# Kernel tuning notes

Measured on AMD Instinct MI355X. Metric: run time of the kernel, lower is better.

## Reference

```python
import jax, jax.numpy as jnp
import numpy as np
import math

D_MSA, N_HEAD, D_HID = 256, 8, 32
B, N, L = 1, 256, 384


def _xavier(key, shape):
    fan_in, fan_out = shape[1], shape[0]
    a = math.sqrt(6.0 / (fan_in + fan_out))
    return jax.random.uniform(key, shape, jnp.float32, -a, a)


def setup_inputs() -> dict:
    key = jax.random.key(0)
    ks = jax.random.split(key, 8)
    hd = N_HEAD * D_HID
    return {
        "msa": jax.random.normal(ks[0], (B, N, L, D_MSA), jnp.float32),
        "ln_w": jnp.ones((D_MSA,), jnp.float32),
        "ln_b": jnp.zeros((D_MSA,), jnp.float32),
        # torch Linear weight is [out, in]; y = x @ W.T
        "wq": _xavier(ks[1], (hd, D_MSA)),
        "wk": _xavier(ks[2], (hd, D_MSA)),
        "wv": _xavier(ks[3], (hd, D_MSA)),
        # to_g init: zeros weight, ones bias -> randomize a bit for nontrivial test
        "wg": 0.02 * jax.random.normal(ks[4], (hd, D_MSA), jnp.float32),
        "bg": jnp.ones((hd,), jnp.float32),
        "wo": 0.02 * jax.random.normal(ks[5], (D_MSA, hd), jnp.float32),
        "bo": jnp.zeros((D_MSA,), jnp.float32),
    }


def reference(msa, ln_w, ln_b, wq, wk, wv, wg, bg, wo, bo):
    h, d = N_HEAD, D_HID
    scaling = 1.0 / math.sqrt(d)
    b, n, l, dm = msa.shape

    # LayerNorm over last dim
    mu = jnp.mean(msa, axis=-1, keepdims=True)
    var = jnp.var(msa, axis=-1, keepdims=True)
    x = (msa - mu) / jnp.sqrt(var + 1e-5) * ln_w + ln_b

    q = (x @ wq.T).reshape(b, n, l, h, d) * scaling
    k = (x @ wk.T).reshape(b, n, l, h, d)
    v = (x @ wv.T).reshape(b, n, l, h, d)
    gate = jax.nn.sigmoid(x @ wg.T + bg)  # [b,n,l,h*d]

    # column-wise attention: softmax over MSA sequence axis N (keys)
    attn = jnp.einsum("bqihd,bkihd->bihqk", q, k)  # [b,l,h,n,n]
    attn = jax.nn.softmax(attn, axis=-1)
    out = jnp.einsum("bihqk,bkihd->bqihd", attn, v).reshape(b, n, l, h * d)
    out = gate * out
    return out @ wo.T + bo
```

## Files before the change

### kernel.cpp

```cpp
#include <hip/hip_runtime.h>

typedef unsigned short u16;
typedef unsigned int u32;
typedef __attribute__((ext_vector_type(8))) short bf16x8;
typedef __attribute__((ext_vector_type(4))) float f32x4;
typedef __attribute__((ext_vector_type(4))) u32 u32x4;

#define N_SEQ 256
#define L_RES 384
#define DM 256
#define NH 8
#define DH 32
#define M_ROWS (N_SEQ*L_RES)
#define PANEL 8192


__device__ __forceinline__ u16 f2b(float f){
    unsigned u = __builtin_bit_cast(unsigned, f);
    u = u + 0x7fffu + ((u >> 16) & 1u);
    return (u16)(u >> 16);
}
__device__ __forceinline__ float b2f(u16 b){
    unsigned u = ((unsigned)b) << 16;
    return __builtin_bit_cast(float, u);
}
__device__ __forceinline__ u32 pk2(float lo, float hi){
    u32 a = (__builtin_bit_cast(u32, lo) + 0x8000u) >> 16;
    u32 b = (__builtin_bit_cast(u32, hi) + 0x8000u) & 0xffff0000u;
    return a | b;
}
__device__ __forceinline__ int swzB(int a){
    return a ^ (((a>>6)&7)<<3);
}

__global__ __launch_bounds__(256) void k_wcvt(const float* __restrict__ wq,
        const float* __restrict__ wk, const float* __restrict__ wv,
        const float* __restrict__ wg, const float* __restrict__ wo,
        u16* __restrict__ wsw){
    const int mat = blockIdx.x >> 6;
    const float* W = (mat==0)?wq:(mat==1)?wk:(mat==2)?wv:(mat==3)?wg:wo;
    const int r = ((blockIdx.x & 63)*256 + threadIdx.x)*4;
    const int col = r >> 8, k0 = r & 255;
    float4 f = *(const float4*)&W[r];
    ushort4 o;
    o.x = f2b(f.x); o.y = f2b(f.y); o.z = f2b(f.z); o.w = f2b(f.w);
    const int off = ((col>>4)*32 + (k0>>3))*128 + (col&15)*8 + (k0&7);
    *(ushort4*)&wsw[mat*65536 + off] = o;
}

__global__ __launch_bounds__(256) void k_ln(const float* __restrict__ msa,
        const float* __restrict__ lnw, const float* __restrict__ lnb,
        u16* __restrict__ xo){
    const int tid = threadIdx.x;
    const int r16 = tid >> 4, lane16 = tid & 15;
    const size_t row = (size_t)blockIdx.x*16 + r16;
    const float4* src = (const float4*)(msa + row*DM + lane16*16);
    float4 a[4];
    float s = 0.f, ss = 0.f;
    #pragma unroll
    for(int j=0;j<4;j++){
        a[j] = src[j];
        s  += a[j].x + a[j].y + a[j].z + a[j].w;
        ss += a[j].x*a[j].x + a[j].y*a[j].y + a[j].z*a[j].z + a[j].w*a[j].w;
    }
    #pragma unroll
    for(int m=1;m<16;m<<=1){ s += __shfl_xor(s,m); ss += __shfl_xor(ss,m); }
    const float mu  = s*(1.f/DM);
    const float inv = rsqrtf(ss*(1.f/DM) - mu*mu + 1e-5f);
    const float4* wv4 = (const float4*)(lnw + lane16*16);
    const float4* bv4 = (const float4*)(lnb + lane16*16);
    u32 pk[8];
    #pragma unroll
    for(int j=0;j<4;j++){
        float4 w = wv4[j], b = bv4[j];
        float e0 = (a[j].x-mu)*inv*w.x + b.x;
        float e1 = (a[j].y-mu)*inv*w.y + b.y;
        float e2 = (a[j].z-mu)*inv*w.z + b.z;
        float e3 = (a[j].w-mu)*inv*w.w + b.w;
        pk[j*2]   = (u32)f2b(e0) | ((u32)f2b(e1)<<16);
        pk[j*2+1] = (u32)f2b(e2) | ((u32)f2b(e3)<<16);
    }
    u16* base = xo + (size_t)blockIdx.x*4096 + lane16*256 + r16*8;
    *(uint4*)base       = *(uint4*)&pk[0];
    *(uint4*)(base+128) = *(uint4*)&pk[4];
}

__global__ __launch_bounds__(512) void k_qkvg(const u16* __restrict__ x,
        const u16* __restrict__ wsw, const float* __restrict__ bg,
        u16* __restrict__ qo, u16* __restrict__ ko,
        u16* __restrict__ vo, u16* __restrict__ go){
    __shared__ __align__(16) u16 Bs[16384];
    const int by = blockIdx.x, mat = blockIdx.y;
    const int tid = threadIdx.x;
    const int w = tid>>6, lane = tid&63, l15 = lane&15, lq = lane>>4;
    const u16* xa = x + ((size_t)by*8 + w)*4096;
    bf16x8 xf[8];
    #pragma unroll
    for(int kk=0;kk<8;kk++)
        xf[kk] = *(const bf16x8*)&xa[(kk*4+lq)*128 + l15*8];
    const float scaling = 0.17677669529663687f * 1.44269504088896f;
    u16* O = (mat==0)?qo:(mat==1)?ko:(mat==2)?vo:go;
    const int n0 = by/3, l0 = (by%3)*128;
    const int l = l0 + w*16 + l15;
    #pragma unroll 1
    for(int cg=0; cg<4; ++cg){
        const u16* wt = wsw + mat*65536 + cg*16384;
        __syncthreads();
        #pragma unroll
        for(int i=0;i<4;i++)
            *(uint4*)&Bs[swzB(i*4096 + tid*8)] = *(const uint4*)&wt[i*4096 + tid*8];
        __syncthreads();
        f32x4 acc[4] = {};
        #pragma unroll
        for(int kk=0;kk<8;kk++){
            #pragma unroll
            for(int nt=0;nt<4;nt++){
                bf16x8 b = *(const bf16x8*)&Bs[swzB(nt*4096 + (kk*4+lq)*128 + l15*8)];
                acc[nt] = __builtin_amdgcn_mfma_f32_16x16x32_bf16(b,xf[kk],acc[nt],0,0,0);
            }
        }
        #pragma unroll
        for(int nt=0;nt<4;nt++){
            const int c = cg*64 + nt*16 + lq*4;
            float v0 = acc[nt][0], v1 = acc[nt][1];
            float v2 = acc[nt][2], v3 = acc[nt][3];
            if(mat==0){ v0*=scaling; v1*=scaling; v2*=scaling; v3*=scaling; }
            else if(mat==3){
                const float4 bgv = *(const float4*)&bg[c];
                v0 = 1.f/(1.f+__expf(-(v0+bgv.x)));
                v1 = 1.f/(1.f+__expf(-(v1+bgv.y)));
                v2 = 1.f/(1.f+__expf(-(v2+bgv.z)));
                v3 = 1.f/(1.f+__expf(-(v3+bgv.w)));
            }
            uint2 ov;
            ov.x = pk2(v0, v1);
            ov.y = pk2(v2, v3);
            const int h2 = c >> 5, d = c & 31;
            *(uint2*)&O[((size_t)l*NH + h2)*PANEL + n0*32 + d] = ov;
        }
    }
}

__global__ __launch_bounds__(512, 4) void k_attn(const u16* __restrict__ q,
        const u16* __restrict__ k, const u16* __restrict__ v,
        const u16* __restrict__ g, u16* __restrict__ ao){
    __shared__ __align__(16) u16 KFs[8192];
    __shared__ __align__(16) u16 VFs[8192];
    const int h = blockIdx.x, l = blockIdx.y;
    const int tid = threadIdx.x;
    const size_t pbase = ((size_t)l*NH + h)*PANEL;
    const u16* kp = k + pbase;
    const u16* vp = v + pbase;
    #pragma unroll
    for(int j=0;j<2;j++){
        const int u = j*512 + tid;
        const int key = u>>2, dblk = u&3;
        const uint4 tk = *(const uint4*)&kp[u*8];
        *(uint4*)&KFs[((key>>4)*4 + dblk)*128 + (key&15)*8] = tk;
        const uint4 tv = *(const uint4*)&vp[u*8];
        const int T = key>>4, gg = (key>>2)&3, r = key&3;
        const int pkey = (T>>1)*32 + ((gg&2)|(T&1))*8 + r + (((gg^T)&1)<<2);
        const int plo = (pkey>>3)*128 + (pkey&7);
        const u32 wv_[4] = {tv.x, tv.y, tv.z, tv.w};
        #pragma unroll
        for(int wd=0; wd<4; wd++){
            const int d_lo = dblk*8 + wd*2, d_hi = d_lo+1;
            VFs[((d_lo)>>4)*4096 + plo + ((d_lo)&15)*8] = (u16)(wv_[wd]&0xffff);
            VFs[((d_hi)>>4)*4096 + plo + ((d_hi)&15)*8] = (u16)(wv_[wd]>>16);
        }
    }
    __syncthreads();
    const int w = tid>>6, lane = tid&63;
    const int l15 = lane&15, lq = lane>>4;
    const int lodd = lq & 1;
    const u16* qp = q + pbase;
    const u16* gp = g + pbase;
    u16* aop = ao + pbase;
    const int q0a = w*32, q0b = w*32 + 16;
    const bf16x8 bqA = *(const bf16x8*)&qp[(q0a+l15)*32 + lq*8];
    const bf16x8 bqB = *(const bf16x8*)&qp[(q0b+l15)*32 + lq*8];
    float mA = -1e30f, spA = 0.f;
    float mB = -1e30f, spB = 0.f;
    f32x4 oaccA[2] = {}, oaccB[2] = {};
    #pragma unroll
    for(int ch=0; ch<4; ch++){
        f32x4 sA[4], sB[4];
        #pragma unroll
        for(int tt=0;tt<4;tt++){
            bf16x8 ak = *(const bf16x8*)&KFs[((ch*4+tt)*4 + lq)*128 + l15*8];
            f32x4 z = {};
            sA[tt] = __builtin_amdgcn_mfma_f32_16x16x32_bf16(ak,bqA,z,0,0,0);
            f32x4 z2 = {};
            sB[tt] = __builtin_amdgcn_mfma_f32_16x16x32_bf16(ak,bqB,z2,0,0,0);
        }
        float cmA = fmaxf(fmaxf(fmaxf(sA[0][0],sA[0][1]),fmaxf(sA[0][2],sA[0][3])),
                   fmaxf(fmaxf(fmaxf(sA[1][0],sA[1][1]),fmaxf(sA[1][2],sA[1][3])),
                   fmaxf(fmaxf(fmaxf(sA[2][0],sA[2][1]),fmaxf(sA[2][2],sA[2][3])),
                         fmaxf(fmaxf(sA[3][0],sA[3][1]),fmaxf(sA[3][2],sA[3][3])))));
        float cmB = fmaxf(fmaxf(fmaxf(sB[0][0],sB[0][1]),fmaxf(sB[0][2],sB[0][3])),
                   fmaxf(fmaxf(fmaxf(sB[1][0],sB[1][1]),fmaxf(sB[1][2],sB[1][3])),
                   fmaxf(fmaxf(fmaxf(sB[2][0],sB[2][1]),fmaxf(sB[2][2],sB[2][3])),
                         fmaxf(fmaxf(sB[3][0],sB[3][1]),fmaxf(sB[3][2],sB[3][3])))));
        cmA = fmaxf(cmA, __shfl_xor(cmA,16));
        cmB = fmaxf(cmB, __shfl_xor(cmB,16));
        cmA = fmaxf(cmA, __shfl_xor(cmA,32));
        cmB = fmaxf(cmB, __shfl_xor(cmB,32));
        if(!__all((cmA <= mA + 8.f) && (cmB <= mB + 8.f))){
            const float mnA = fmaxf(mA, cmA), mnB = fmaxf(mB, cmB);
            const float scA = exp2f(mA - mnA), scB = exp2f(mB - mnB);
            mA = mnA; mB = mnB;
            spA *= scA; spB *= scB;
            #pragma unroll
            for(int i=0;i<4;i++){ oaccA[0][i]*=scA; oaccA[1][i]*=scA; oaccB[0][i]*=scB; oaccB[1][i]*=scB; }
        }
        float csA = 0.f, csB = 0.f;
        #pragma unroll
        for(int tt=0;tt<4;tt++){
            #pragma unroll
            for(int rg=0;rg<4;rg++){
                float eA = exp2f(sA[tt][rg] - mA);
                float eB = exp2f(sB[tt][rg] - mB);
                sA[tt][rg] = eA; csA += eA;
                sB[tt][rg] = eB; csB += eB;
            }
        }
        spA += csA;
        spB += csB;
        #pragma unroll
        for(int half=0; half<2; half++){
            const int mwin = ch*2 + half;
            u32 eA0 = pk2(sA[half*2][0],   sA[half*2][1]);
            u32 eA1 = pk2(sA[half*2][2],   sA[half*2][3]);
            u32 oA0 = pk2(sA[half*2+1][0], sA[half*2+1][1]);
            u32 oA1 = pk2(sA[half*2+1][2], sA[half*2+1][3]);
            u32 eB0 = pk2(sB[half*2][0],   sB[half*2][1]);
            u32 eB1 = pk2(sB[half*2][2],   sB[half*2][3]);
            u32 oB0 = pk2(sB[half*2+1][0], sB[half*2+1][1]);
            u32 oB1 = pk2(sB[half*2+1][2], sB[half*2+1][3]);
            u32 ownA0 = lodd ? oA0 : eA0,  ownA1 = lodd ? oA1 : eA1;
            u32 sndA0 = lodd ? eA0 : oA0,  sndA1 = lodd ? eA1 : oA1;
            u32 ownB0 = lodd ? oB0 : eB0,  ownB1 = lodd ? oB1 : eB1;
            u32 sndB0 = lodd ? eB0 : oB0,  sndB1 = lodd ? eB1 : oB1;
            u32 rcA0 = (u32)__shfl_xor((int)sndA0, 16);
            u32 rcB0 = (u32)__shfl_xor((int)sndB0, 16);
            u32 rcA1 = (u32)__shfl_xor((int)sndA1, 16);
            u32 rcB1 = (u32)__shfl_xor((int)sndB1, 16);
            u32x4 pwA = {ownA0, ownA1, rcA0, rcA1};
            u32x4 pwB = {ownB0, ownB1, rcB0, rcB1};
            bf16x8 pfA = __builtin_bit_cast(bf16x8, pwA);
            bf16x8 pfB = __builtin_bit_cast(bf16x8, pwB);
            #pragma unroll
            for(int nt=0;nt<2;nt++){
                bf16x8 av = *(const bf16x8*)&VFs[(nt*32 + mwin*4 + lq)*128 + l15*8];
                oaccA[nt] = __builtin_amdgcn_mfma_f32_16x16x32_bf16(av,pfA,oaccA[nt],0,0,0);
                oaccB[nt] = __builtin_amdgcn_mfma_f32_16x16x32_bf16(av,pfB,oaccB[nt],0,0,0);
            }
        }
    }
    spA += __shfl_xor(spA, 16);
    spB += __shfl_xor(spB, 16);
    spA += __shfl_xor(spA, 32);
    spB += __shfl_xor(spB, 32);
    const float rinvA = 1.f/spA, rinvB = 1.f/spB;
    const int qnA = q0a + l15, qnB = q0b + l15;
    #pragma unroll
    for(int nt=0;nt<2;nt++){
        const int c = nt*16 + lq*4;
        const uint2 glA = *(const uint2*)&gp[qnA*32 + c];
        const uint2 glB = *(const uint2*)&gp[qnB*32 + c];
        uint2 ovA, ovB;
        ovA.x = pk2(b2f((u16)(glA.x&0xffff))*oaccA[nt][0]*rinvA,
                    b2f((u16)(glA.x>>16))   *oaccA[nt][1]*rinvA);
        ovA.y = pk2(b2f((u16)(glA.y&0xffff))*oaccA[nt][2]*rinvA,
                    b2f((u16)(glA.y>>16))   *oaccA[nt][3]*rinvA);
        ovB.x = pk2(b2f((u16)(glB.x&0xffff))*oaccB[nt][0]*rinvB,
                    b2f((u16)(glB.x>>16))   *oaccB[nt][1]*rinvB);
        ovB.y = pk2(b2f((u16)(glB.y&0xffff))*oaccB[nt][2]*rinvB,
                    b2f((u16)(glB.y>>16))   *oaccB[nt][3]*rinvB);
        *(uint2*)&aop[qnA*32 + c] = ovA;
        *(uint2*)&aop[qnB*32 + c] = ovB;
    }
}

__global__ __launch_bounds__(512) void k_out(const u16* __restrict__ a,
        const u16* __restrict__ wsw, const float* __restrict__ bo,
        float* __restrict__ out){
    __shared__ __align__(16) u16 Bs[16384];
    const int cb = blockIdx.x, nb = blockIdx.y, l = blockIdx.z;
    const int c0 = cb*64;
    const int tid = threadIdx.x;
    const u16* wt = wsw + 4*65536 + (c0>>4)*4096;
    #pragma unroll
    for(int i=0;i<4;i++)
        *(uint4*)&Bs[swzB(i*4096 + tid*8)] = *(const uint4*)&wt[i*4096 + tid*8];
    const int w = tid>>6, lane = tid&63, l15 = lane&15, lq = lane>>4;
    const int n0 = nb*128 + w*16;
    const size_t lbase = (size_t)l*NH*PANEL;
    bf16x8 af[8];
    #pragma unroll
    for(int kk=0;kk<8;kk++)
        af[kk] = *(const bf16x8*)&a[lbase + (size_t)kk*PANEL + (n0 + l15)*32 + lq*8];
    __syncthreads();
    f32x4 acc[4] = {};
    #pragma unroll
    for(int kk=0;kk<8;kk++){
        #pragma unroll
        for(int nt=0;nt<4;nt++){
            bf16x8 b = *(const bf16x8*)&Bs[swzB(nt*4096 + (kk*4+lq)*128 + l15*8)];
            acc[nt] = __builtin_amdgcn_mfma_f32_16x16x32_bf16(af[kk],b,acc[nt],0,0,0);
        }
    }
    #pragma unroll
    for(int nt=0;nt<4;nt++){
        const int c = c0 + nt*16 + l15;
        const float bov = bo[c];
        #pragma unroll
        for(int rg=0;rg<4;rg++){
            const int n = n0 + lq*4 + rg;
            out[((size_t)n*L_RES + l)*DM + c] = acc[nt][rg] + bov;
        }
    }
}

extern "C" void kernel_launch(void* const* d_in, const int* in_sizes, int n_in,
                              void* d_out, int out_size, void* d_ws, size_t ws_size,
                              hipStream_t stream){
    const float* msa = (const float*)d_in[0];
    const float* lnw = (const float*)d_in[1];
    const float* lnb = (const float*)d_in[2];
    const float* wq  = (const float*)d_in[3];
    const float* wk  = (const float*)d_in[4];
    const float* wv  = (const float*)d_in[5];
    const float* wg  = (const float*)d_in[6];
    const float* bg  = (const float*)d_in[7];
    const float* wo  = (const float*)d_in[8];
    const float* bo  = (const float*)d_in[9];
    float* out = (float*)d_out;

    const size_t SEG = (size_t)M_ROWS * DM;
    u16 *xs, *qs, *ks, *vs, *gs, *aos, *wsw;
    if (ws_size >= (6*SEG + 5*65536) * sizeof(u16)) {
        xs  = (u16*)d_ws;
        qs  = xs + SEG;
        ks  = qs + SEG;
        vs  = ks + SEG;
        gs  = vs + SEG;
        aos = gs + SEG;
        wsw = aos + SEG;
    } else {
        xs  = (u16*)d_ws;
        qs  = xs + SEG;
        gs  = qs + SEG;
        wsw = gs + SEG;
        ks  = (u16*)d_out;
        vs  = ks + SEG;
        aos = xs;
    }

    k_wcvt<<<320, 256, 0, stream>>>(wq, wk, wv, wg, wo, wsw);
    k_ln  <<<M_ROWS/16, 256, 0, stream>>>(msa, lnw, lnb, xs);
    k_qkvg<<<dim3(M_ROWS/128, 4), 512, 0, stream>>>(xs, wsw, bg, qs, ks, vs, gs);
    k_attn<<<dim3(NH, L_RES), 512, 0, stream>>>(qs, ks, vs, gs, aos);
    k_out <<<dim3(4, 2, L_RES), 512, 0, stream>>>(aos, wsw, bo, out);
}
```

Measured before the change: 277.0 us.

## Fuse LayerNorm into QKVG projection kernel and loop over matrices per block

Removes the standalone LayerNorm kernel. The projection kernel now reads fp32 msa rows directly, computes mean and variance with wave shuffles, and builds bf16 MFMA operands in registers. Each block then loops over all four weight matrices instead of using a grid dimension per matrix. This drops the bf16 intermediate round-trip through global memory and one launch. In exchange the grid is four times smaller with longer-running blocks, which reduces parallelism and latency hiding.

```diff
diff --git a/kernel.cpp b/kernel.cpp
--- a/kernel.cpp
+++ b/kernel.cpp
@@ -48,95 +48,88 @@
     *(ushort4*)&wsw[mat*65536 + off] = o;
 }
 
-__global__ __launch_bounds__(256) void k_ln(const float* __restrict__ msa,
+__global__ __launch_bounds__(512) void k_lnqkvg(const float* __restrict__ msa,
         const float* __restrict__ lnw, const float* __restrict__ lnb,
-        u16* __restrict__ xo){
-    const int tid = threadIdx.x;
-    const int r16 = tid >> 4, lane16 = tid & 15;
-    const size_t row = (size_t)blockIdx.x*16 + r16;
-    const float4* src = (const float4*)(msa + row*DM + lane16*16);
-    float4 a[4];
-    float s = 0.f, ss = 0.f;
-    #pragma unroll
-    for(int j=0;j<4;j++){
-        a[j] = src[j];
-        s  += a[j].x + a[j].y + a[j].z + a[j].w;
-        ss += a[j].x*a[j].x + a[j].y*a[j].y + a[j].z*a[j].z + a[j].w*a[j].w;
-    }
-    #pragma unroll
-    for(int m=1;m<16;m<<=1){ s += __shfl_xor(s,m); ss += __shfl_xor(ss,m); }
-    const float mu  = s*(1.f/DM);
-    const float inv = rsqrtf(ss*(1.f/DM) - mu*mu + 1e-5f);
-    const float4* wv4 = (const float4*)(lnw + lane16*16);
-    const float4* bv4 = (const float4*)(lnb + lane16*16);
-    u32 pk[8];
-    #pragma unroll
-    for(int j=0;j<4;j++){
-        float4 w = wv4[j], b = bv4[j];
-        float e0 = (a[j].x-mu)*inv*w.x + b.x;
-        float e1 = (a[j].y-mu)*inv*w.y + b.y;
-        float e2 = (a[j].z-mu)*inv*w.z + b.z;
-        float e3 = (a[j].w-mu)*inv*w.w + b.w;
-        pk[j*2]   = (u32)f2b(e0) | ((u32)f2b(e1)<<16);
-        pk[j*2+1] = (u32)f2b(e2) | ((u32)f2b(e3)<<16);
-    }
-    u16* base = xo + (size_t)blockIdx.x*4096 + lane16*256 + r16*8;
-    *(uint4*)base       = *(uint4*)&pk[0];
-    *(uint4*)(base+128) = *(uint4*)&pk[4];
-}
-
-__global__ __launch_bounds__(512) void k_qkvg(const u16* __restrict__ x,
         const u16* __restrict__ wsw, const float* __restrict__ bg,
         u16* __restrict__ qo, u16* __restrict__ ko,
         u16* __restrict__ vo, u16* __restrict__ go){
     __shared__ __align__(16) u16 Bs[16384];
-    const int by = blockIdx.x, mat = blockIdx.y;
+    const int by = blockIdx.x;
     const int tid = threadIdx.x;
     const int w = tid>>6, lane = tid&63, l15 = lane&15, lq = lane>>4;
-    const u16* xa = x + ((size_t)by*8 + w)*4096;
+    const size_t row = (size_t)by*128 + w*16 + l15;
+    const float* mrow = msa + row*DM;
+    float4 f0[8], f1[8];
+    float s = 0.f, ss = 0.f;
+    #pragma unroll
+    for(int kk=0;kk<8;kk++){
+        const float4* p = (const float4*)&mrow[(kk*4+lq)*8];
+        f0[kk] = p[0]; f1[kk] = p[1];
+        s  += f0[kk].x+f0[kk].y+f0[kk].z+f0[kk].w + f1[kk].x+f1[kk].y+f1[kk].z+f1[kk].w;
+        ss += f0[kk].x*f0[kk].x+f0[kk].y*f0[kk].y+f0[kk].z*f0[kk].z+f0[kk].w*f0[kk].w
+            + f1[kk].x*f1[kk].x+f1[kk].y*f1[kk].y+f1[kk].z*f1[kk].z+f1[kk].w*f1[kk].w;
+    }
+    s  += __shfl_xor(s,16);  s  += __shfl_xor(s,32);
+    ss += __shfl_xor(ss,16); ss += __shfl_xor(ss,32);
+    const float mu  = s*(1.f/DM);
+    const float inv = rsqrtf(ss*(1.f/DM) - mu*mu + 1e-5f);
     bf16x8 xf[8];
     #pragma unroll
-    for(int kk=0;kk<8;kk++)
-        xf[kk] = *(const bf16x8*)&xa[(kk*4+lq)*128 + l15*8];
+    for(int kk=0;kk<8;kk++){
+        const int c0 = (kk*4+lq)*8;
+        const float4 w0 = *(const float4*)&lnw[c0];
+        const float4 w1 = *(const float4*)&lnw[c0+4];
+        const float4 b0 = *(const float4*)&lnb[c0];
+        const float4 b1 = *(const float4*)&lnb[c0+4];
+        u32x4 pw;
+        pw.x = pk2((f0[kk].x-mu)*inv*w0.x + b0.x, (f0[kk].y-mu)*inv*w0.y + b0.y);
+        pw.y = pk2((f0[kk].z-mu)*inv*w0.z + b0.z, (f0[kk].w-mu)*inv*w0.w + b0.w);
+        pw.z = pk2((f1[kk].x-mu)*inv*w1.x + b1.x, (f1[kk].y-mu)*inv*w1.y + b1.y);
+        pw.w = pk2((f1[kk].z-mu)*inv*w1.z + b1.z, (f1[kk].w-mu)*inv*w1.w + b1.w);
+        xf[kk] = __builtin_bit_cast(bf16x8, pw);
+    }
     const float scaling = 0.17677669529663687f * 1.44269504088896f;
-    u16* O = (mat==0)?qo:(mat==1)?ko:(mat==2)?vo:go;
     const int n0 = by/3, l0 = (by%3)*128;
     const int l = l0 + w*16 + l15;
     #pragma unroll 1
-    for(int cg=0; cg<4; ++cg){
-        const u16* wt = wsw + mat*65536 + cg*16384;
-        __syncthreads();
-        #pragma unroll
-        for(int i=0;i<4;i++)
-            *(uint4*)&Bs[swzB(i*4096 + tid*8)] = *(const uint4*)&wt[i*4096 + tid*8];
-        __syncthreads();
-        f32x4 acc[4] = {};
-        #pragma unroll
-        for(int kk=0;kk<8;kk++){
+    for(int mat=0; mat<4; ++mat){
+        u16* O = (mat==0)?qo:(mat==1)?ko:(mat==2)?vo:go;
+        #pragma unroll 1
+        for(int cg=0; cg<4; ++cg){
+            const u16* wt = wsw + mat*65536 + cg*16384;
+            __syncthreads();
+            #pragma unroll
+            for(int i=0;i<4;i++)
+                *(uint4*)&Bs[swzB(i*4096 + tid*8)] = *(const uint4*)&wt[i*4096 + tid*8];
+            __syncthreads();
+            f32x4 acc[4] = {};
+            #pragma unroll
+            for(int kk=0;kk<8;kk++){
+                #pragma unroll
+                for(int nt=0;nt<4;nt++){
+                    bf16x8 b = *(const bf16x8*)&Bs[swzB(nt*4096 + (kk*4+lq)*128 + l15*8)];
+                    acc[nt] = __builtin_amdgcn_mfma_f32_16x16x32_bf16(b,xf[kk],acc[nt],0,0,0);
+                }
+            }
             #pragma unroll
             for(int nt=0;nt<4;nt++){
-                bf16x8 b = *(const bf16x8*)&Bs[swzB(nt*4096 + (kk*4+lq)*128 + l15*8)];
-                acc[nt] = __builtin_amdgcn_mfma_f32_16x16x32_bf16(b,xf[kk],acc[nt],0,0,0);
+                const int c = cg*64 + nt*16 + lq*4;
+                float v0 = acc[nt][0], v1 = acc[nt][1];
+                float v2 = acc[nt][2], v3 = acc[nt][3];
+                if(mat==0){ v0*=scaling; v1*=scaling; v2*=scaling; v3*=scaling; }
+                else if(mat==3){
+                    const float4 bgv = *(const float4*)&bg[c];
+                    v0 = 1.f/(1.f+__expf(-(v0+bgv.x)));
+                    v1 = 1.f/(1.f+__expf(-(v1+bgv.y)));
+                    v2 = 1.f/(1.f+__expf(-(v2+bgv.z)));
+                    v3 = 1.f/(1.f+__expf(-(v3+bgv.w)));
+                }
+                uint2 ov;
+                ov.x = pk2(v0, v1);
+                ov.y = pk2(v2, v3);
+                const int h2 = c >> 5, d = c & 31;
+                *(uint2*)&O[((size_t)l*NH + h2)*PANEL + n0*32 + d] = ov;
             }
-        }
-        #pragma unroll
-        for(int nt=0;nt<4;nt++){
-            const int c = cg*64 + nt*16 + lq*4;
-            float v0 = acc[nt][0], v1 = acc[nt][1];
-            float v2 = acc[nt][2], v3 = acc[nt][3];
-            if(mat==0){ v0*=scaling; v1*=scaling; v2*=scaling; v3*=scaling; }
-            else if(mat==3){
-                const float4 bgv = *(const float4*)&bg[c];
-                v0 = 1.f/(1.f+__expf(-(v0+bgv.x)));
-                v1 = 1.f/(1.f+__expf(-(v1+bgv.y)));
-                v2 = 1.f/(1.f+__expf(-(v2+bgv.z)));
-                v3 = 1.f/(1.f+__expf(-(v3+bgv.w)));
-            }
-            uint2 ov;
-            ov.x = pk2(v0, v1);
-            ov.y = pk2(v2, v3);
-            const int h2 = c >> 5, d = c & 31;
-            *(uint2*)&O[((size_t)l*NH + h2)*PANEL + n0*32 + d] = ov;
         }
     }
 }
@@ -357,9 +350,8 @@
         aos = xs;
     }
 
-    k_wcvt<<<320, 256, 0, stream>>>(wq, wk, wv, wg, wo, wsw);
-    k_ln  <<<M_ROWS/16, 256, 0, stream>>>(msa, lnw, lnb, xs);
-    k_qkvg<<<dim3(M_ROWS/128, 4), 512, 0, stream>>>(xs, wsw, bg, qs, ks, vs, gs);
-    k_attn<<<dim3(NH, L_RES), 512, 0, stream>>>(qs, ks, vs, gs, aos);
-    k_out <<<dim3(4, 2, L_RES), 512, 0, stream>>>(aos, wsw, bo, out);
-}
+    k_wcvt  <<<320, 256, 0, stream>>>(wq, wk, wv, wg, wo, wsw);
+    k_lnqkvg<<<M_ROWS/128, 512, 0, stream>>>(msa, lnw, lnb, wsw, bg, qs, ks, vs, gs);
+    k_attn  <<<dim3(NH, L_RES), 512, 0, stream>>>(qs, ks, vs, gs, aos);
+    k_out   <<<dim3(4, 2, L_RES), 512, 0, stream>>>(aos, wsw, bo, out);
+}
```

Result: slower. 283.5 us (+2.3%).
